# Performance work log

Hardware: AMD Instinct MI355X
Metric: run time of the kernel (lower is better)

The kernel has to match this reference:

```python
import jax, jax.numpy as jnp
import numpy as np

D = 128  # d_pair
N = 512  # n_res
B = 1
EPS = 1e-5


def setup_inputs() -> dict:
    key = jax.random.key(0)
    ks = jax.random.split(key, 16)
    s = 0.02
    inp = {
        "pair": jax.random.normal(ks[0], (B, N, N, D), dtype=jnp.float32),
        "pair_mask": jnp.ones((B, N, N), dtype=jnp.float32),
        "ln_g": jnp.ones((D,), dtype=jnp.float32),
        "ln_b": jnp.zeros((D,), dtype=jnp.float32),
        "w_lp": jax.random.normal(ks[1], (D, D), dtype=jnp.float32) * s,
        "b_lp": jnp.zeros((D,), dtype=jnp.float32),
        "w_lg": jax.random.normal(ks[2], (D, D), dtype=jnp.float32) * s,
        "b_lg": jnp.zeros((D,), dtype=jnp.float32),
        "w_rp": jax.random.normal(ks[3], (D, D), dtype=jnp.float32) * s,
        "b_rp": jnp.zeros((D,), dtype=jnp.float32),
        "w_rg": jax.random.normal(ks[4], (D, D), dtype=jnp.float32) * s,
        "b_rg": jnp.zeros((D,), dtype=jnp.float32),
        "w_g": jax.random.normal(ks[5], (D, D), dtype=jnp.float32) * s,
        "b_g": jnp.zeros((D,), dtype=jnp.float32),
        "w_o": jax.random.normal(ks[6], (D, D), dtype=jnp.float32) * s,
        "b_o": jnp.zeros((D,), dtype=jnp.float32),
    }
    return inp


def _layer_norm(x, g, b):
    mu = jnp.mean(x, axis=-1, keepdims=True)
    var = jnp.mean(jnp.square(x - mu), axis=-1, keepdims=True)
    return (x - mu) * jax.lax.rsqrt(var + EPS) * g + b


def reference(pair, pair_mask, ln_g, ln_b, w_lp, b_lp, w_lg, b_lg,
              w_rp, b_rp, w_rg, b_rg, w_g, b_g, w_o, b_o):
    # [B,N,N,D] pair representation; outgoing triangle multiplication
    x = _layer_norm(pair, ln_g, ln_b)
    mask = pair_mask[..., None]  # [B,N,N,1]
    left = (x @ w_lp + b_lp) * jax.nn.sigmoid(x @ w_lg + b_lg) * mask
    right = (x @ w_rp + b_rp) * jax.nn.sigmoid(x @ w_rg + b_rg) * mask
    # outgoing: contract over j -> per-channel NxN matmul
    out = jnp.einsum('bijd,bjkd->bikd', left, right)
    out = out * jax.nn.sigmoid(x @ w_g + b_g)
    out = out @ w_o + b_o
    return out
```

## Files before the change

kernel.cpp:

```cpp
#include <hip/hip_runtime.h>

#define NN 512
#define DD 128
#define PP (NN*NN)

typedef __attribute__((ext_vector_type(8))) short short8;
typedef __attribute__((ext_vector_type(4))) float floatx4;
typedef __attribute__((ext_vector_type(4))) unsigned int uintx4;
typedef __attribute__((ext_vector_type(2))) unsigned int uintx2;

__device__ __forceinline__ unsigned short f2bf(float f) {
  unsigned int u = __float_as_uint(f);
  u += 0x7fffu + ((u >> 16) & 1u);
  return (unsigned short)(u >> 16);
}
__device__ __forceinline__ float bf2f(unsigned short h) {
  return __uint_as_float(((unsigned int)h) << 16);
}
__device__ __forceinline__ unsigned int pkbf2(float lo, float hi) {
  unsigned int r;
  asm("v_cvt_pk_bf16_f32 %0, %1, %2" : "=v"(r) : "v"(lo), "v"(hi));
  return r;
}
__device__ __forceinline__ float sigm(float x) {
  return 1.f / (1.f + __expf(-x));
}

__device__ __forceinline__ void gload_lds16(const unsigned short* g, unsigned short* l) {
  __builtin_amdgcn_global_load_lds(
      (const __attribute__((address_space(1))) unsigned int*)g,
      (__attribute__((address_space(3))) unsigned int*)l, 16, 0, 0);
}

__global__ void k0_prep(const float* __restrict__ wlp, const float* __restrict__ wlg,
                        const float* __restrict__ wrp, const float* __restrict__ wrg,
                        const float* __restrict__ wg,  const float* __restrict__ wo,
                        unsigned short* __restrict__ wt) {
  const float* src[6] = {wlp, wlg, wrp, wrg, wg, wo};
  int m = blockIdx.y;
  int idx = blockIdx.x * 256 + threadIdx.x;
  int d = idx >> 7, e = idx & 127;
  wt[m * 16384 + e * 128 + d] = f2bf(src[m][d * 128 + e]);
}

__launch_bounds__(256, 8)
__global__ void k1a_ln(const float* __restrict__ pair,
                       const float* __restrict__ lng, const float* __restrict__ lnb,
                       unsigned short* __restrict__ xln) {
  const int t = threadIdx.x;
  const int sub = t & 31;
  const long row0 = (long)blockIdx.x * 128 + (t >> 5);
  const floatx4 g4 = *(const floatx4*)(lng + sub * 4);
  const floatx4 b4 = *(const floatx4*)(lnb + sub * 4);
  const float* src = pair + row0 * DD + sub * 4;
  unsigned short* dst = xln + row0 * DD + sub * 4;
  floatx4 vn = *(const floatx4*)src;
  #pragma unroll
  for (int pass = 0; pass < 16; ++pass) {
    floatx4 v = vn;
    if (pass < 15) vn = *(const floatx4*)(src + (pass + 1) * 8 * DD);
    float s  = v.x + v.y + v.z + v.w;
    float s2 = v.x * v.x + v.y * v.y + v.z * v.z + v.w * v.w;
    #pragma unroll
    for (int m = 1; m < 32; m <<= 1) {
      s  += __shfl_xor(s, m);
      s2 += __shfl_xor(s2, m);
    }
    float mu = s * (1.f / 128.f);
    float rs = rsqrtf(s2 * (1.f / 128.f) - mu * mu + 1e-5f);
    uintx2 o;
    o[0] = pkbf2((v.x - mu) * rs * g4.x + b4.x, (v.y - mu) * rs * g4.y + b4.y);
    o[1] = pkbf2((v.z - mu) * rs * g4.z + b4.z, (v.w - mu) * rs * g4.w + b4.w);
    *(uintx2*)(dst + pass * 8 * DD) = o;
  }
}

__launch_bounds__(512, 4)
__global__ void k1b_proj(const unsigned short* __restrict__ xln,
                         const float* __restrict__ pmask,
                         const unsigned short* __restrict__ wt,
                         const float* __restrict__ b_lp, const float* __restrict__ b_lg,
                         const float* __restrict__ b_rp, const float* __restrict__ b_rg,
                         const float* __restrict__ b_g,
                         unsigned short* __restrict__ left_t,
                         unsigned short* __restrict__ right_bt,
                         unsigned short* __restrict__ gate_t) {
  __shared__ __align__(16) unsigned short Sm[24576];
  __shared__ float Mlds[128];

  const int t = threadIdx.x;
  const int unit = blockIdx.y;
  const int q = blockIdx.x;

  int j0 = 0, kk = 0;
  long p0 = 0, soff;
  if (unit == 1) {
    j0 = (q >> 9) << 7; kk = q & 511;
    soff = (long)kk * NN + j0;
  } else {
    p0 = (long)q << 7;
    soff = p0;
  }
  auto arow = [&](int r) -> long {
    return (unit == 1) ? ((long)(j0 + r) * NN + kk) : (p0 + r);
  };

  if (unit < 2 && t < 128) Mlds[t] = pmask[arow(t)];

  const unsigned short* wA = wt + (unit == 0 ? 0 : unit == 1 ? 2 : 4) * 16384;
  const unsigned short* wB = wt + (unit == 0 ? 1 : 3) * 16384;

  const int lane = t & 63, w = t >> 6;
  const int ln = lane & 15, q8 = lane >> 4;
  const int wm = (w >> 2) << 6, we = (w & 3) << 5;
  const int sr = t >> 2, sc = t & 3;

  const long aBase = arow(sr) * DD + sc * 8;

  auto STAGE = [&](int set, int kc) {
    unsigned short* base = Sm + set * 12288;
    gload_lds16(xln + aBase + kc * 32,            &base[t * 8]);
    gload_lds16(wA + sr * 128 + kc * 32 + sc * 8, &base[4096 + t * 8]);
    if (unit < 2)
      gload_lds16(wB + sr * 128 + kc * 32 + sc * 8, &base[8192 + t * 8]);
  };

  floatx4 aP[4][2] = {}, aG[4][2] = {};
  STAGE(0, 0);
  __syncthreads();
  #pragma unroll
  for (int kc = 0; kc < 4; ++kc) {
    const int cur = kc & 1;
    if (kc < 3) STAGE(cur ^ 1, kc + 1);
    unsigned short* Al = Sm + cur * 12288;
    unsigned short* Bp = Al + 4096;
    unsigned short* Bg = Al + 8192;
    short8 a[4];
    #pragma unroll
    for (int i = 0; i < 4; ++i)
      a[i] = *(const short8*)&Al[(wm + i * 16 + ln) * 32 + q8 * 8];
    #pragma unroll
    for (int j = 0; j < 2; ++j) {
      short8 bpv = *(const short8*)&Bp[(we + j * 16 + ln) * 32 + q8 * 8];
      #pragma unroll
      for (int i = 0; i < 4; ++i)
        aP[i][j] = __builtin_amdgcn_mfma_f32_16x16x32_bf16(a[i], bpv, aP[i][j], 0, 0, 0);
    }
    if (unit < 2) {
      #pragma unroll
      for (int j = 0; j < 2; ++j) {
        short8 bgv = *(const short8*)&Bg[(we + j * 16 + ln) * 32 + q8 * 8];
        #pragma unroll
        for (int i = 0; i < 4; ++i)
          aG[i][j] = __builtin_amdgcn_mfma_f32_16x16x32_bf16(a[i], bgv, aG[i][j], 0, 0, 0);
      }
    }
    __syncthreads();
  }

  unsigned short* mystg = Sm + w * 2176;
  if (unit < 2) {
    const float* bpp = (unit == 0) ? b_lp : b_rp;
    const float* bgg = (unit == 0) ? b_lg : b_rg;
    #pragma unroll
    for (int j = 0; j < 2; ++j) {
      int eg = we + j * 16 + ln;
      float bp = bpp[eg], bg = bgg[eg];
      #pragma unroll
      for (int i = 0; i < 4; ++i) {
        float vv[4];
        #pragma unroll
        for (int r = 0; r < 4; ++r) {
          int m = wm + i * 16 + q8 * 4 + r;
          vv[r] = (aP[i][j][r] + bp) * sigm(aG[i][j][r] + bg) * Mlds[m];
        }
        unsigned int* du = (unsigned int*)&mystg[(j * 16 + ln) * 68 + i * 16 + q8 * 4];
        du[0] = pkbf2(vv[0], vv[1]);
        du[1] = pkbf2(vv[2], vv[3]);
      }
    }
  } else {
    #pragma unroll
    for (int j = 0; j < 2; ++j) {
      int eg = we + j * 16 + ln;
      float bg = b_g[eg];
      #pragma unroll
      for (int i = 0; i < 4; ++i) {
        float vv[4];
        #pragma unroll
        for (int r = 0; r < 4; ++r)
          vv[r] = sigm(aP[i][j][r] + bg);
        unsigned int* du = (unsigned int*)&mystg[(j * 16 + ln) * 68 + i * 16 + q8 * 4];
        du[0] = pkbf2(vv[0], vv[1]);
        du[1] = pkbf2(vv[2], vv[3]);
      }
    }
  }

  unsigned short* dstbase = (unit == 0) ? left_t : (unit == 1 ? right_bt : gate_t);
  #pragma unroll
  for (int itr = 0; itr < 4; ++itr) {
    int row = itr * 8 + (lane >> 3);
    int c = lane & 7;
    short8 vv = *(const short8*)&mystg[row * 68 + c * 8];
    long eg = we + row;
    *(short8*)(dstbase + eg * PP + soff + wm + c * 8) = vv;
  }
}

__launch_bounds__(512, 4)
__global__ void k2_einsum(const unsigned short* __restrict__ left_t,
                          const unsigned short* __restrict__ right_bt,
                          const unsigned short* __restrict__ gate_t,
                          unsigned short* __restrict__ tmpg) {
  __shared__ __align__(16) unsigned short Sm[16896];
  unsigned short* Cl = Sm;
  const int t = threadIdx.x;
  const int d = blockIdx.y;
  const int i0 = (blockIdx.x >> 2) << 7;
  const int k0 = (blockIdx.x & 3) << 7;
  const unsigned short* Ag = left_t   + (long)d * PP;
  const unsigned short* Bg = right_bt + (long)d * PP;
  const unsigned short* Gg = gate_t   + (long)d * PP;
  const int lane = t & 63, w = t >> 6;
  const int ln = lane & 15, q8 = lane >> 4;
  const int wm = (w >> 2) << 6, wn = (w & 3) << 5;
  const int sr = t >> 2, sc = t & 3;

  const long aBase = (long)(i0 + sr) * NN + sc * 8;
  const long bBase = (long)(k0 + sr) * NN + sc * 8;

  auto STAGE = [&](int set, int jj) {
    gload_lds16(Ag + aBase + jj, &Sm[set * 8192 + t * 8]);
    gload_lds16(Bg + bBase + jj, &Sm[set * 8192 + 4096 + t * 8]);
  };

  floatx4 acc[4][2] = {};
  STAGE(0, 0);
  __syncthreads();
  for (int it = 0; it < 16; ++it) {
    const int cur = it & 1;
    if (it < 15) STAGE(cur ^ 1, (it + 1) * 32);
    unsigned short* Al = Sm + cur * 8192;
    unsigned short* Bl = Al + 4096;
    short8 a[4], b[2];
    #pragma unroll
    for (int i = 0; i < 4; ++i)
      a[i] = *(const short8*)&Al[(wm + i * 16 + ln) * 32 + q8 * 8];
    #pragma unroll
    for (int j = 0; j < 2; ++j)
      b[j] = *(const short8*)&Bl[(wn + j * 16 + ln) * 32 + q8 * 8];
    #pragma unroll
    for (int i = 0; i < 4; ++i)
      #pragma unroll
      for (int j = 0; j < 2; ++j)
        acc[i][j] = __builtin_amdgcn_mfma_f32_16x16x32_bf16(a[i], b[j], acc[i][j], 0, 0, 0);
    __syncthreads();
  }
  #pragma unroll
  for (int i = 0; i < 4; ++i)
    #pragma unroll
    for (int j = 0; j < 2; ++j) {
      int n = wn + j * 16 + ln;
      #pragma unroll
      for (int r = 0; r < 4; ++r) {
        int m = wm + i * 16 + q8 * 4 + r;
        float gf = bf2f(Gg[(long)(i0 + m) * NN + k0 + n]);
        Cl[m * 132 + n] = f2bf(acc[i][j][r] * gf);
      }
    }
  __syncthreads();
  unsigned short* Og = tmpg + (long)d * PP;
  #pragma unroll
  for (int it = 0; it < 4; ++it) {
    int flat = it * 512 + t;
    int m = flat >> 4, c = flat & 15;
    *(short8*)(Og + (long)(i0 + m) * NN + k0 + c * 8) = *(const short8*)&Cl[m * 132 + c * 8];
  }
}

__launch_bounds__(512, 4)
__global__ void k3_out(const unsigned short* __restrict__ tmpg,
                       const unsigned short* __restrict__ wt,
                       const float* __restrict__ b_o,
                       float* __restrict__ out) {
  __shared__ __align__(16) unsigned short Tl[128 * 144];
  unsigned int* TlU = (unsigned int*)Tl;
  const int t = threadIdx.x;
  const long p0 = (long)blockIdx.x << 7;
  const unsigned short* wo = wt + 5 * 16384;

  #pragma unroll
  for (int it = 0; it < 2; ++it) {
    int flat = it * 512 + t;
    int rp = flat >> 4;
    int c  = flat & 15;
    const unsigned short* ra = tmpg + (long)(2 * rp) * PP + p0 + c * 8;
    uintx4 xa = *(const uintx4*)ra;
    uintx4 xb = *(const uintx4*)(ra + PP);
    int sw = ((c & 7) << 3) ^ ((c >> 3) << 2);
    #pragma unroll
    for (int cc = 0; cc < 4; ++cc) {
      int p = c * 8 + 2 * cc;
      TlU[p * 72 + (rp ^ sw)]       = (xa[cc] & 0xffffu) | (xb[cc] << 16);
      TlU[(p + 1) * 72 + (rp ^ sw)] = (xa[cc] >> 16) | (xb[cc] & 0xffff0000u);
    }
  }
  __syncthreads();

  const int lane = t & 63, w = t >> 6;
  const int ln = lane & 15, q8 = lane >> 4;
  const int wm = (w >> 2) << 6, wn = (w & 3) << 5;

  floatx4 acc[4][2] = {};
  #pragma unroll
  for (int ks = 0; ks < 4; ++ks) {
    short8 a[4], b[2];
    #pragma unroll
    for (int i = 0; i < 4; ++i) {
      int p = wm + i * 16 + ln;
      int swh = (((p >> 3) & 7) << 4) ^ (((p >> 6) & 1) << 3);
      a[i] = *(const short8*)&Tl[p * 144 + ((ks * 32 + q8 * 8) ^ swh)];
    }
    #pragma unroll
    for (int j = 0; j < 2; ++j)
      b[j] = *(const short8*)(wo + (wn + j * 16 + ln) * 128 + ks * 32 + q8 * 8);
    #pragma unroll
    for (int i = 0; i < 4; ++i)
      #pragma unroll
      for (int j = 0; j < 2; ++j)
        acc[i][j] = __builtin_amdgcn_mfma_f32_16x16x32_bf16(a[i], b[j], acc[i][j], 0, 0, 0);
  }
  #pragma unroll
  for (int j = 0; j < 2; ++j) {
    int eg = wn + j * 16 + ln;
    float bias = b_o[eg];
    #pragma unroll
    for (int i = 0; i < 4; ++i)
      #pragma unroll
      for (int r = 0; r < 4; ++r) {
        int m = wm + i * 16 + q8 * 4 + r;
        out[(p0 + m) * DD + eg] = acc[i][j][r] + bias;
      }
  }
}

extern "C" void kernel_launch(void* const* d_in, const int* in_sizes, int n_in,
                              void* d_out, int out_size, void* d_ws, size_t ws_size,
                              hipStream_t stream) {
  const float* pair = (const float*)d_in[0];
  const float* pmask = (const float*)d_in[1];
  const float* ln_g = (const float*)d_in[2];
  const float* ln_b = (const float*)d_in[3];
  const float* w_lp = (const float*)d_in[4];
  const float* b_lp = (const float*)d_in[5];
  const float* w_lg = (const float*)d_in[6];
  const float* b_lg = (const float*)d_in[7];
  const float* w_rp = (const float*)d_in[8];
  const float* b_rp = (const float*)d_in[9];
  const float* w_rg = (const float*)d_in[10];
  const float* b_rg = (const float*)d_in[11];
  const float* w_g  = (const float*)d_in[12];
  const float* b_g  = (const float*)d_in[13];
  const float* w_o  = (const float*)d_in[14];
  const float* b_o  = (const float*)d_in[15];
  float* out = (float*)d_out;

  char* ws = (char*)d_ws;
  unsigned short* wt       = (unsigned short*)ws;
  unsigned short* xln      = (unsigned short*)(ws + 196608);
  unsigned short* left_t   = xln      + (size_t)PP * DD;
  unsigned short* right_bt = left_t   + (size_t)PP * DD;
  unsigned short* gate_t   = right_bt + (size_t)PP * DD;
  unsigned short* tmpg     = xln;

  k0_prep<<<dim3(64, 6), 256, 0, stream>>>(w_lp, w_lg, w_rp, w_rg, w_g, w_o, wt);
  k1a_ln<<<dim3(2048), 256, 0, stream>>>(pair, ln_g, ln_b, xln);
  k1b_proj<<<dim3(2048, 3), 512, 0, stream>>>(xln, pmask, wt,
      b_lp, b_lg, b_rp, b_rg, b_g, left_t, right_bt, gate_t);
  k2_einsum<<<dim3(16, 128), 512, 0, stream>>>(left_t, right_bt, gate_t, tmpg);
  k3_out<<<dim3(2048), 512, 0, stream>>>(tmpg, wt, b_o, out);
}
```

Measured before the change: 488.7 us.

## Fuse LayerNorm into projection GEMM by folding mean/scale into epilogue

Removes the standalone LayerNorm kernel and its bf16 intermediate buffer. The projection kernel now reads fp32 pair rows directly, computes per-row mean and rstd, and stores x*gamma into swizzled LDS. The mean and scale corrections are applied in the GEMM epilogue through precomputed gamma·W and beta·W+bias vectors. Weights are now read straight from global memory instead of being staged in LDS. The trade-off is that each fp32 pair row is reloaded by all three projection units, and computing on uncentered x*gamma in bf16 can lose precision relative to centering first.

```diff
diff --git a/kernel.cpp b/kernel.cpp
--- a/kernel.cpp
+++ b/kernel.cpp
@@ -8,6 +8,9 @@
 typedef __attribute__((ext_vector_type(4))) float floatx4;
 typedef __attribute__((ext_vector_type(4))) unsigned int uintx4;
 typedef __attribute__((ext_vector_type(2))) unsigned int uintx2;
+
+__device__ float g_gw[640];
+__device__ float g_bwt[640];
 
 __device__ __forceinline__ unsigned short f2bf(float f) {
   unsigned int u = __float_as_uint(f);
@@ -43,50 +46,37 @@
   wt[m * 16384 + e * 128 + d] = f2bf(src[m][d * 128 + e]);
 }
 
-__launch_bounds__(256, 8)
-__global__ void k1a_ln(const float* __restrict__ pair,
-                       const float* __restrict__ lng, const float* __restrict__ lnb,
-                       unsigned short* __restrict__ xln) {
-  const int t = threadIdx.x;
-  const int sub = t & 31;
-  const long row0 = (long)blockIdx.x * 128 + (t >> 5);
-  const floatx4 g4 = *(const floatx4*)(lng + sub * 4);
-  const floatx4 b4 = *(const floatx4*)(lnb + sub * 4);
-  const float* src = pair + row0 * DD + sub * 4;
-  unsigned short* dst = xln + row0 * DD + sub * 4;
-  floatx4 vn = *(const floatx4*)src;
-  #pragma unroll
-  for (int pass = 0; pass < 16; ++pass) {
-    floatx4 v = vn;
-    if (pass < 15) vn = *(const floatx4*)(src + (pass + 1) * 8 * DD);
-    float s  = v.x + v.y + v.z + v.w;
-    float s2 = v.x * v.x + v.y * v.y + v.z * v.z + v.w * v.w;
-    #pragma unroll
-    for (int m = 1; m < 32; m <<= 1) {
-      s  += __shfl_xor(s, m);
-      s2 += __shfl_xor(s2, m);
-    }
-    float mu = s * (1.f / 128.f);
-    float rs = rsqrtf(s2 * (1.f / 128.f) - mu * mu + 1e-5f);
-    uintx2 o;
-    o[0] = pkbf2((v.x - mu) * rs * g4.x + b4.x, (v.y - mu) * rs * g4.y + b4.y);
-    o[1] = pkbf2((v.z - mu) * rs * g4.z + b4.z, (v.w - mu) * rs * g4.w + b4.w);
-    *(uintx2*)(dst + pass * 8 * DD) = o;
-  }
+__global__ void k0b_gw(const float* __restrict__ lng, const float* __restrict__ lnb,
+                       const unsigned short* __restrict__ wt,
+                       const float* __restrict__ b_lp, const float* __restrict__ b_lg,
+                       const float* __restrict__ b_rp, const float* __restrict__ b_rg,
+                       const float* __restrict__ b_g) {
+  int m = blockIdx.x;
+  int e = threadIdx.x;
+  const unsigned short* wcol = wt + m * 16384 + e * 128;
+  float sg = 0.f, sb = 0.f;
+  for (int d = 0; d < 128; ++d) {
+    float wv = bf2f(wcol[d]);
+    sg += lng[d] * wv;
+    sb += lnb[d] * wv;
+  }
+  const float* bias = (m == 0) ? b_lp : (m == 1) ? b_lg : (m == 2) ? b_rp
+                      : (m == 3) ? b_rg : b_g;
+  g_gw[m * 128 + e] = sg;
+  g_bwt[m * 128 + e] = sb + bias[e];
 }
 
 __launch_bounds__(512, 4)
-__global__ void k1b_proj(const unsigned short* __restrict__ xln,
+__global__ void k1b_proj(const float* __restrict__ pair,
                          const float* __restrict__ pmask,
+                         const float* __restrict__ lng,
                          const unsigned short* __restrict__ wt,
-                         const float* __restrict__ b_lp, const float* __restrict__ b_lg,
-                         const float* __restrict__ b_rp, const float* __restrict__ b_rg,
-                         const float* __restrict__ b_g,
                          unsigned short* __restrict__ left_t,
                          unsigned short* __restrict__ right_bt,
                          unsigned short* __restrict__ gate_t) {
-  __shared__ __align__(16) unsigned short Sm[24576];
-  __shared__ float Mlds[128];
+  __shared__ __align__(16) unsigned short Sm[17408];
+  __shared__ float Rs[128], Rm[128], Mlds[128];
+  unsigned int* AbfU = (unsigned int*)Sm;
 
   const int t = threadIdx.x;
   const int unit = blockIdx.y;
@@ -107,41 +97,51 @@
 
   if (unit < 2 && t < 128) Mlds[t] = pmask[arow(t)];
 
+  const int sub = t & 31;
+  const int rb = t >> 5;
+  const floatx4 g4 = *(const floatx4*)(lng + sub * 4);
+  #pragma unroll
+  for (int pass = 0; pass < 8; ++pass) {
+    int r = rb + 16 * pass;
+    floatx4 v = *(const floatx4*)(pair + arow(r) * DD + sub * 4);
+    float s  = v.x + v.y + v.z + v.w;
+    float s2 = v.x * v.x + v.y * v.y + v.z * v.z + v.w * v.w;
+    #pragma unroll
+    for (int mm = 1; mm < 32; mm <<= 1) {
+      s  += __shfl_xor(s, mm);
+      s2 += __shfl_xor(s2, mm);
+    }
+    float mu = s * (1.f / 128.f);
+    float rs = rsqrtf(s2 * (1.f / 128.f) - mu * mu + 1e-5f);
+    if (sub == 0) { Rs[r] = rs; Rm[r] = rs * mu; }
+    uintx2 o;
+    o[0] = pkbf2(v.x * g4.x, v.y * g4.y);
+    o[1] = pkbf2(v.z * g4.z, v.w * g4.w);
+    int chunk = (sub >> 1) ^ (r & 7);
+    *(uintx2*)&AbfU[r * 64 + chunk * 4 + (sub & 1) * 2] = o;
+  }
+  __syncthreads();
+
   const unsigned short* wA = wt + (unit == 0 ? 0 : unit == 1 ? 2 : 4) * 16384;
   const unsigned short* wB = wt + (unit == 0 ? 1 : 3) * 16384;
 
   const int lane = t & 63, w = t >> 6;
   const int ln = lane & 15, q8 = lane >> 4;
   const int wm = (w >> 2) << 6, we = (w & 3) << 5;
-  const int sr = t >> 2, sc = t & 3;
-
-  const long aBase = arow(sr) * DD + sc * 8;
-
-  auto STAGE = [&](int set, int kc) {
-    unsigned short* base = Sm + set * 12288;
-    gload_lds16(xln + aBase + kc * 32,            &base[t * 8]);
-    gload_lds16(wA + sr * 128 + kc * 32 + sc * 8, &base[4096 + t * 8]);
-    if (unit < 2)
-      gload_lds16(wB + sr * 128 + kc * 32 + sc * 8, &base[8192 + t * 8]);
-  };
 
   floatx4 aP[4][2] = {}, aG[4][2] = {};
-  STAGE(0, 0);
-  __syncthreads();
   #pragma unroll
   for (int kc = 0; kc < 4; ++kc) {
-    const int cur = kc & 1;
-    if (kc < 3) STAGE(cur ^ 1, kc + 1);
-    unsigned short* Al = Sm + cur * 12288;
-    unsigned short* Bp = Al + 4096;
-    unsigned short* Bg = Al + 8192;
     short8 a[4];
     #pragma unroll
-    for (int i = 0; i < 4; ++i)
-      a[i] = *(const short8*)&Al[(wm + i * 16 + ln) * 32 + q8 * 8];
+    for (int i = 0; i < 4; ++i) {
+      int r = wm + i * 16 + ln;
+      int chunk = (kc * 4 + q8) ^ (ln & 7);
+      a[i] = *(const short8*)&Sm[r * 128 + chunk * 8];
+    }
     #pragma unroll
     for (int j = 0; j < 2; ++j) {
-      short8 bpv = *(const short8*)&Bp[(we + j * 16 + ln) * 32 + q8 * 8];
+      short8 bpv = *(const short8*)(wA + (we + j * 16 + ln) * 128 + kc * 32 + q8 * 8);
       #pragma unroll
       for (int i = 0; i < 4; ++i)
         aP[i][j] = __builtin_amdgcn_mfma_f32_16x16x32_bf16(a[i], bpv, aP[i][j], 0, 0, 0);
@@ -149,30 +149,35 @@
     if (unit < 2) {
       #pragma unroll
       for (int j = 0; j < 2; ++j) {
-        short8 bgv = *(const short8*)&Bg[(we + j * 16 + ln) * 32 + q8 * 8];
+        short8 bgv = *(const short8*)(wB + (we + j * 16 + ln) * 128 + kc * 32 + q8 * 8);
         #pragma unroll
         for (int i = 0; i < 4; ++i)
           aG[i][j] = __builtin_amdgcn_mfma_f32_16x16x32_bf16(a[i], bgv, aG[i][j], 0, 0, 0);
       }
     }
-    __syncthreads();
-  }
+  }
+  __syncthreads();
 
   unsigned short* mystg = Sm + w * 2176;
   if (unit < 2) {
-    const float* bpp = (unit == 0) ? b_lp : b_rp;
-    const float* bgg = (unit == 0) ? b_lg : b_rg;
+    const float* gwP = g_gw  + (unit * 2) * 128;
+    const float* bwP = g_bwt + (unit * 2) * 128;
+    const float* gwG = g_gw  + (unit * 2 + 1) * 128;
+    const float* bwG = g_bwt + (unit * 2 + 1) * 128;
     #pragma unroll
     for (int j = 0; j < 2; ++j) {
       int eg = we + j * 16 + ln;
-      float bp = bpp[eg], bg = bgg[eg];
+      float gp = gwP[eg], bp = bwP[eg], gg = gwG[eg], bg = bwG[eg];
       #pragma unroll
       for (int i = 0; i < 4; ++i) {
         float vv[4];
         #pragma unroll
         for (int r = 0; r < 4; ++r) {
           int m = wm + i * 16 + q8 * 4 + r;
-          vv[r] = (aP[i][j][r] + bp) * sigm(aG[i][j][r] + bg) * Mlds[m];
+          float rs = Rs[m], rm = Rm[m];
+          float vp = rs * aP[i][j][r] - rm * gp + bp;
+          float vg = rs * aG[i][j][r] - rm * gg + bg;
+          vv[r] = vp * sigm(vg) * Mlds[m];
         }
         unsigned int* du = (unsigned int*)&mystg[(j * 16 + ln) * 68 + i * 16 + q8 * 4];
         du[0] = pkbf2(vv[0], vv[1]);
@@ -180,16 +185,20 @@
       }
     }
   } else {
+    const float* gw4 = g_gw  + 4 * 128;
+    const float* bw4 = g_bwt + 4 * 128;
     #pragma unroll
     for (int j = 0; j < 2; ++j) {
       int eg = we + j * 16 + ln;
-      float bg = b_g[eg];
+      float gp = gw4[eg], bp = bw4[eg];
       #pragma unroll
       for (int i = 0; i < 4; ++i) {
         float vv[4];
         #pragma unroll
-        for (int r = 0; r < 4; ++r)
-          vv[r] = sigm(aP[i][j][r] + bg);
+        for (int r = 0; r < 4; ++r) {
+          int m = wm + i * 16 + q8 * 4 + r;
+          vv[r] = sigm(Rs[m] * aP[i][j][r] - Rm[m] * gp + bp);
+        }
         unsigned int* du = (unsigned int*)&mystg[(j * 16 + ln) * 68 + i * 16 + q8 * 4];
         du[0] = pkbf2(vv[0], vv[1]);
         du[1] = pkbf2(vv[2], vv[3]);
@@ -368,16 +377,15 @@
 
   char* ws = (char*)d_ws;
   unsigned short* wt       = (unsigned short*)ws;
-  unsigned short* xln      = (unsigned short*)(ws + 196608);
-  unsigned short* left_t   = xln      + (size_t)PP * DD;
+  unsigned short* tmpg     = (unsigned short*)(ws + 196608);
+  unsigned short* left_t   = tmpg     + (size_t)PP * DD;
   unsigned short* right_bt = left_t   + (size_t)PP * DD;
   unsigned short* gate_t   = right_bt + (size_t)PP * DD;
-  unsigned short* tmpg     = xln;
 
   k0_prep<<<dim3(64, 6), 256, 0, stream>>>(w_lp, w_lg, w_rp, w_rg, w_g, w_o, wt);
-  k1a_ln<<<dim3(2048), 256, 0, stream>>>(pair, ln_g, ln_b, xln);
-  k1b_proj<<<dim3(2048, 3), 512, 0, stream>>>(xln, pmask, wt,
-      b_lp, b_lg, b_rp, b_rg, b_g, left_t, right_bt, gate_t);
+  k0b_gw<<<dim3(5), 128, 0, stream>>>(ln_g, ln_b, wt, b_lp, b_lg, b_rp, b_rg, b_g);
+  k1b_proj<<<dim3(2048, 3), 512, 0, stream>>>(pair, pmask, ln_g, wt,
+      left_t, right_bt, gate_t);
   k2_einsum<<<dim3(16, 128), 512, 0, stream>>>(left_t, right_bt, gate_t, tmpg);
   k3_out<<<dim3(2048), 512, 0, stream>>>(tmpg, wt, b_o, out);
 }
```

Measured after the change: 566.8 us. 1.16x slower.
